# Kernel optimization log

Measured on AMD Instinct MI355X. Metric: run time of the kernel, lower is better.

## Reference

```python
import jax, jax.numpy as jnp
import numpy as np
import math

NUM_BLOCKS = 8
SPARSITY_THRESHOLD = 0.01
HARD_FRAC = 1.0
HIDDEN_SIZE = 1024
HIDDEN_FACTOR = 2
SCALE = 0.02


def _dht1d(x, axis):
    # Discrete Hartley transform along `axis`: sum x * cas(2*pi*k*n/N)
    # cas = cos + sin, equivalently Re(FFT) - Im(FFT).
    F = jnp.fft.fft(x, axis=axis)
    return F.real - F.imag


def dht2d(x):
    # Separable 2D Hartley transform over the spatial axes (1, 2) of (B,H,W,C).
    return _dht1d(_dht1d(x, 1), 2)


def setup_inputs() -> dict:
    key = jax.random.key(0)
    k_x, k_w1, k_b1, k_w2, k_b2 = jax.random.split(key, 5)
    B, N, C = 4, 16384, HIDDEN_SIZE
    bs = C // NUM_BLOCKS                      # 128
    hid = bs * HIDDEN_FACTOR                  # 256
    x = jax.random.normal(k_x, (B, N, C), dtype=jnp.float32)
    w1 = SCALE * jax.random.normal(k_w1, (2, NUM_BLOCKS, bs, hid), dtype=jnp.float32)
    b1 = SCALE * jax.random.normal(k_b1, (2, NUM_BLOCKS, hid), dtype=jnp.float32)
    w2 = SCALE * jax.random.normal(k_w2, (2, NUM_BLOCKS, hid, bs), dtype=jnp.float32)
    b2 = SCALE * jax.random.normal(k_b2, (2, NUM_BLOCKS, bs), dtype=jnp.float32)
    return {"x": x, "w1": w1, "b1": b1, "w2": w2, "b2": b2}


def reference(x, w1, b1, w2, b2):
    bias = x
    B, N, C = x.shape
    H = W = int(math.sqrt(N))
    bs = C // NUM_BLOCKS

    xs = x.reshape(B, H, W, C)
    xs = dht2d(xs)                                    # spatial Hartley domain
    xs = xs.reshape(B, H, W, NUM_BLOCKS, bs)

    kept = int(math.sqrt(H * W) * HARD_FRAC)          # = H when frac == 1
    xk = xs[:, :kept, :kept]                          # (B, kept, kept, nb, bs)

    # Block-diagonal spectral MLP; the source sums contributions from both
    # weight slices w[0] and w[1] with bias b[0].
    o1 = jax.nn.relu(
        jnp.einsum("bxyni,nio->bxyno", xk, w1[0])
        + jnp.einsum("bxyni,nio->bxyno", xk, w1[1])
        + b1[0]
    )                                                 # (B, kept, kept, nb, hid)
    o2k = (
        jnp.einsum("bxyno,noi->bxyni", o1, w2[0])
        + jnp.einsum("bxyno,noi->bxyni", o1, w2[1])
        + b2[0]
    )                                                 # (B, kept, kept, nb, bs)

    o2 = jnp.zeros_like(xs).at[:, :kept, :kept].set(o2k)

    # softshrink
    lam = jnp.float32(SPARSITY_THRESHOLD)
    z = jnp.sign(o2) * jax.nn.relu(jnp.abs(o2) - lam)

    z = z.reshape(B, H, W, C)
    z = dht2d(z) / (H * W)                            # inverse Hartley
    return z.reshape(B, N, C) + bias
```

## Files before the change

### kernel.cpp

```cpp
#include <hip/hip_runtime.h>

typedef unsigned short u16;
typedef unsigned int   u32;
typedef __attribute__((ext_vector_type(8))) short bf16x8;
typedef __attribute__((ext_vector_type(4))) short bf16x4;
typedef __attribute__((ext_vector_type(4))) float f32x4;

#define LAM 0.01f

__device__ __forceinline__ u16 f2bf(float f){
  u32 u = __float_as_uint(f);
  u = u + 0x7FFFu + ((u >> 16) & 1u);
  return (u16)(u >> 16);
}

__device__ __forceinline__ int swz(int row, int k){
  return row*128 + ((((k >> 3) ^ row) & 15) << 3) + (k & 7);
}

#define MFMA16(ac, a, b) ac = __builtin_amdgcn_mfma_f32_16x16x32_bf16((a), (b), (ac), 0, 0, 0)

#define GEMM_STEP(acc, A0,A1,A2,A3, B0,B1,B2,B3) \
  MFMA16(acc[0], A0,B0); MFMA16(acc[1], A0,B1); MFMA16(acc[2], A0,B2); MFMA16(acc[3], A0,B3); \
  MFMA16(acc[4], A1,B0); MFMA16(acc[5], A1,B1); MFMA16(acc[6], A1,B2); MFMA16(acc[7], A1,B3); \
  MFMA16(acc[8], A2,B0); MFMA16(acc[9], A2,B1); MFMA16(acc[10],A2,B2); MFMA16(acc[11],A2,B3); \
  MFMA16(acc[12],A3,B0); MFMA16(acc[13],A3,B1); MFMA16(acc[14],A3,B2); MFMA16(acc[15],A3,B3);

__global__ void k_prep(const float* __restrict__ w1, const float* __restrict__ w2,
                       u16* __restrict__ Mg, u16* __restrict__ W1et, u16* __restrict__ W2et){
  int gid = blockIdx.x * 256 + threadIdx.x;
  if (gid < 16384){
    int i = gid >> 7, j = gid & 127;
    int t = (i * j) & 127;
    float ang = (float)t * 0.04908738521234052f;
    Mg[gid] = f2bf(cosf(ang) + sinf(ang));
  } else if (gid < 16384 + 262144){
    int e = gid - 16384;
    int n = e >> 15, o = (e >> 7) & 255, i = e & 127;
    float v = w1[(n*128 + i)*256 + o] + w1[((8+n)*128 + i)*256 + o];
    W1et[e] = f2bf(v);
  } else {
    int e = gid - (16384 + 262144);
    int n = e >> 15, i = (e >> 8) & 127, o = e & 255;
    float v = w2[(n*256 + o)*128 + i] + w2[((8+n)*256 + o)*128 + i];
    W2et[e] = f2bf(v);
  }
}

__launch_bounds__(256, 2)
__global__ void k_dht_fwd(const float* __restrict__ x, const u16* __restrict__ Mg,
                          u16* __restrict__ Ag){
  __shared__ u16 xt[128*128];
  __shared__ u16 st[128*128];
  int bi = blockIdx.x;
  int n = bi & 7, w = (bi >> 3) & 127, b = bi >> 10;
  int tid = threadIdx.x;
  int lane = tid & 63, wid = tid >> 6;
  int l15 = lane & 15, q = lane >> 4;
  int r0 = (wid >> 1) * 64, c0 = (wid & 1) * 64;

  {
    int c = tid & 127, hg = tid >> 7;
    const float* xb = x + ((b*128)*128 + w)*1024 + n*128 + c;
    for (int it = 0; it < 32; ++it){
      int h0 = (hg + 2*it) * 2;
      float v0 = xb[h0 * 131072];
      float v1 = xb[(h0+1) * 131072];
      u32 pk = (u32)f2bf(v0) | ((u32)f2bf(v1) << 16);
      *(u32*)(&xt[swz(c, h0)]) = pk;
    }
  }
  __syncthreads();

  f32x4 acc[16];
#pragma unroll
  for (int t = 0; t < 16; ++t) acc[t] = f32x4{0.f,0.f,0.f,0.f};

#pragma unroll
  for (int ks = 0; ks < 4; ++ks){
    int kk = ks*32 + q*8;
    bf16x8 a0 = *(const bf16x8*)(Mg + (r0 +  0 + l15)*128 + kk);
    bf16x8 a1 = *(const bf16x8*)(Mg + (r0 + 16 + l15)*128 + kk);
    bf16x8 a2 = *(const bf16x8*)(Mg + (r0 + 32 + l15)*128 + kk);
    bf16x8 a3 = *(const bf16x8*)(Mg + (r0 + 48 + l15)*128 + kk);
    bf16x8 b0 = *(const bf16x8*)(&xt[swz(c0 +  0 + l15, kk)]);
    bf16x8 b1 = *(const bf16x8*)(&xt[swz(c0 + 16 + l15, kk)]);
    bf16x8 b2 = *(const bf16x8*)(&xt[swz(c0 + 32 + l15, kk)]);
    bf16x8 b3 = *(const bf16x8*)(&xt[swz(c0 + 48 + l15, kk)]);
    GEMM_STEP(acc, a0,a1,a2,a3, b0,b1,b2,b3);
  }

#pragma unroll
  for (int i = 0; i < 4; ++i){
    int rb = r0 + 16*i + q*4;
#pragma unroll
    for (int j = 0; j < 4; ++j){
      int col = c0 + 16*j + l15;
      f32x4 v = acc[i*4+j];
      st[swz(rb+0, col)] = f2bf(v.x);
      st[swz(rb+1, col)] = f2bf(v.y);
      st[swz(rb+2, col)] = f2bf(v.z);
      st[swz(rb+3, col)] = f2bf(v.w);
    }
  }
  __syncthreads();
  u16* Aout = Ag + ((b*128)*128 + w)*1024 + n*128;
#pragma unroll
  for (int it = 0; it < 8; ++it){
    int cid = it*256 + tid;
    int row = cid >> 4, cp = cid & 15;
    bf16x8 v = *(const bf16x8*)(&st[row*128 + (((cp ^ row) & 15) << 3)]);
    *(bf16x8*)(Aout + row*131072 + cp*8) = v;
  }
}

__launch_bounds__(256, 2)
__global__ void k_mlp(const u16* __restrict__ Xg, const u16* __restrict__ W1et,
                      const u16* __restrict__ W2et, const u16* __restrict__ Mg,
                      const float* __restrict__ b1g, const float* __restrict__ b2g,
                      u16* __restrict__ Ug){
  __shared__ u16 bufA[128*128];
  __shared__ u16 bufB[128*128];
  int bi = blockIdx.x;
  int n = bi & 7, h = (bi >> 3) & 127, b = bi >> 10;
  int tid = threadIdx.x;
  int lane = tid & 63, wid = tid >> 6;
  int l15 = lane & 15, q = lane >> 4;
  int r0 = (wid >> 1) * 64, c0 = (wid & 1) * 64;

  const u16*  Xbase  = Xg + ((b*128 + h)*128)*1024 + n*128;
  const u16*  W1base = W1et + n*256*128;
  const u16*  W2base = W2et + n*128*256;
  const float* b1base = b1g + n*256;
  const float* b2base = b2g + n*128;

  f32x4 acc2[16], acc1[16];
#pragma unroll
  for (int t = 0; t < 16; ++t) acc2[t] = f32x4{0.f,0.f,0.f,0.f};

  for (int half = 0; half < 2; ++half){
#pragma unroll
    for (int t = 0; t < 16; ++t) acc1[t] = f32x4{0.f,0.f,0.f,0.f};
#pragma unroll
    for (int ks = 0; ks < 4; ++ks){
      int kk = ks*32 + q*8;
      bf16x8 a0 = *(const bf16x8*)(Xbase + (r0 +  0 + l15)*1024 + kk);
      bf16x8 a1 = *(const bf16x8*)(Xbase + (r0 + 16 + l15)*1024 + kk);
      bf16x8 a2 = *(const bf16x8*)(Xbase + (r0 + 32 + l15)*1024 + kk);
      bf16x8 a3 = *(const bf16x8*)(Xbase + (r0 + 48 + l15)*1024 + kk);
      const u16* wb = W1base + (half*128 + c0 + l15)*128 + kk;
      bf16x8 b0 = *(const bf16x8*)(wb);
      bf16x8 b1 = *(const bf16x8*)(wb + 16*128);
      bf16x8 b2 = *(const bf16x8*)(wb + 32*128);
      bf16x8 b3 = *(const bf16x8*)(wb + 48*128);
      GEMM_STEP(acc1, a0,a1,a2,a3, b0,b1,b2,b3);
    }
#pragma unroll
    for (int i = 0; i < 4; ++i){
      int kw = r0 + 16*i + q*4;
#pragma unroll
      for (int j = 0; j < 4; ++j){
        int row = c0 + 16*j + l15;
        f32x4 v = acc1[i*4+j];
        bf16x4 pk;
        pk.x = (short)f2bf(v.x); pk.y = (short)f2bf(v.y);
        pk.z = (short)f2bf(v.z); pk.w = (short)f2bf(v.w);
        *(bf16x4*)(&bufA[swz(row, kw)]) = pk;
      }
    }
    __syncthreads();

#pragma unroll
    for (int t = 0; t < 16; ++t) acc1[t] = f32x4{0.f,0.f,0.f,0.f};
#pragma unroll
    for (int ks = 0; ks < 4; ++ks){
      int kk = ks*32 + q*8;
      bf16x8 a0 = *(const bf16x8*)(&bufA[swz(r0 +  0 + l15, kk)]);
      bf16x8 a1 = *(const bf16x8*)(&bufA[swz(r0 + 16 + l15, kk)]);
      bf16x8 a2 = *(const bf16x8*)(&bufA[swz(r0 + 32 + l15, kk)]);
      bf16x8 a3 = *(const bf16x8*)(&bufA[swz(r0 + 48 + l15, kk)]);
      bf16x8 b0 = *(const bf16x8*)(Mg + (c0 +  0 + l15)*128 + kk);
      bf16x8 b1 = *(const bf16x8*)(Mg + (c0 + 16 + l15)*128 + kk);
      bf16x8 b2 = *(const bf16x8*)(Mg + (c0 + 32 + l15)*128 + kk);
      bf16x8 b3 = *(const bf16x8*)(Mg + (c0 + 48 + l15)*128 + kk);
      GEMM_STEP(acc1, a0,a1,a2,a3, b0,b1,b2,b3);
    }
#pragma unroll
    for (int i = 0; i < 4; ++i){
      int ko = r0 + 16*i + q*4;
      float bs0 = b1base[half*128 + ko + 0];
      float bs1 = b1base[half*128 + ko + 1];
      float bs2 = b1base[half*128 + ko + 2];
      float bs3 = b1base[half*128 + ko + 3];
#pragma unroll
      for (int j = 0; j < 4; ++j){
        int row = c0 + 16*j + l15;
        f32x4 v = acc1[i*4+j];
        bf16x4 pk;
        pk.x = (short)f2bf(fmaxf(v.x + bs0, 0.f));
        pk.y = (short)f2bf(fmaxf(v.y + bs1, 0.f));
        pk.z = (short)f2bf(fmaxf(v.z + bs2, 0.f));
        pk.w = (short)f2bf(fmaxf(v.w + bs3, 0.f));
        *(bf16x4*)(&bufB[swz(row, ko)]) = pk;
      }
    }
    __syncthreads();

#pragma unroll
    for (int ks = 0; ks < 4; ++ks){
      int kk = ks*32 + q*8;
      bf16x8 a0 = *(const bf16x8*)(&bufB[swz(r0 +  0 + l15, kk)]);
      bf16x8 a1 = *(const bf16x8*)(&bufB[swz(r0 + 16 + l15, kk)]);
      bf16x8 a2 = *(const bf16x8*)(&bufB[swz(r0 + 32 + l15, kk)]);
      bf16x8 a3 = *(const bf16x8*)(&bufB[swz(r0 + 48 + l15, kk)]);
      const u16* wb = W2base + (c0 + l15)*256 + half*128 + kk;
      bf16x8 b0 = *(const bf16x8*)(wb);
      bf16x8 b1 = *(const bf16x8*)(wb + 16*256);
      bf16x8 b2 = *(const bf16x8*)(wb + 32*256);
      bf16x8 b3 = *(const bf16x8*)(wb + 48*256);
      GEMM_STEP(acc2, a0,a1,a2,a3, b0,b1,b2,b3);
    }
    __syncthreads();
  }

  {
    float b2v[4];
#pragma unroll
    for (int j = 0; j < 4; ++j) b2v[j] = b2base[c0 + 16*j + l15];
#pragma unroll
    for (int i = 0; i < 4; ++i){
      int kw = r0 + 16*i + q*4;
#pragma unroll
      for (int j = 0; j < 4; ++j){
        int row = c0 + 16*j + l15;
        f32x4 v = acc2[i*4+j];
        float t0 = v.x + b2v[j], t1 = v.y + b2v[j], t2 = v.z + b2v[j], t3 = v.w + b2v[j];
        float m0 = fmaxf(fabsf(t0) - LAM, 0.f);
        float m1 = fmaxf(fabsf(t1) - LAM, 0.f);
        float m2 = fmaxf(fabsf(t2) - LAM, 0.f);
        float m3 = fmaxf(fabsf(t3) - LAM, 0.f);
        bf16x4 pk;
        pk.x = (short)f2bf(t0 >= 0.f ? m0 : -m0);
        pk.y = (short)f2bf(t1 >= 0.f ? m1 : -m1);
        pk.z = (short)f2bf(t2 >= 0.f ? m2 : -m2);
        pk.w = (short)f2bf(t3 >= 0.f ? m3 : -m3);
        *(bf16x4*)(&bufA[swz(row, kw)]) = pk;
      }
    }
  }
  __syncthreads();

#pragma unroll
  for (int t = 0; t < 16; ++t) acc1[t] = f32x4{0.f,0.f,0.f,0.f};
#pragma unroll
  for (int ks = 0; ks < 4; ++ks){
    int kk = ks*32 + q*8;
    bf16x8 a0 = *(const bf16x8*)(Mg + (r0 +  0 + l15)*128 + kk);
    bf16x8 a1 = *(const bf16x8*)(Mg + (r0 + 16 + l15)*128 + kk);
    bf16x8 a2 = *(const bf16x8*)(Mg + (r0 + 32 + l15)*128 + kk);
    bf16x8 a3 = *(const bf16x8*)(Mg + (r0 + 48 + l15)*128 + kk);
    bf16x8 b0 = *(const bf16x8*)(&bufA[swz(c0 +  0 + l15, kk)]);
    bf16x8 b1 = *(const bf16x8*)(&bufA[swz(c0 + 16 + l15, kk)]);
    bf16x8 b2 = *(const bf16x8*)(&bufA[swz(c0 + 32 + l15, kk)]);
    bf16x8 b3 = *(const bf16x8*)(&bufA[swz(c0 + 48 + l15, kk)]);
    GEMM_STEP(acc1, a0,a1,a2,a3, b0,b1,b2,b3);
  }
#pragma unroll
  for (int i = 0; i < 4; ++i){
    int rb = r0 + 16*i + q*4;
#pragma unroll
    for (int j = 0; j < 4; ++j){
      int col = c0 + 16*j + l15;
      f32x4 v = acc1[i*4+j];
      bufB[swz(rb+0, col)] = f2bf(v.x);
      bufB[swz(rb+1, col)] = f2bf(v.y);
      bufB[swz(rb+2, col)] = f2bf(v.z);
      bufB[swz(rb+3, col)] = f2bf(v.w);
    }
  }
  __syncthreads();
  u16* Ubase = Ug + ((b*128 + h)*128)*1024 + n*128;
#pragma unroll
  for (int it = 0; it < 8; ++it){
    int cid = it*256 + tid;
    int row = cid >> 4, cp = cid & 15;
    bf16x8 v = *(const bf16x8*)(&bufB[row*128 + (((cp ^ row) & 15) << 3)]);
    *(bf16x8*)(Ubase + row*1024 + cp*8) = v;
  }
}

__launch_bounds__(256, 2)
__global__ void k_dht_inv(const u16* __restrict__ Ug, const u16* __restrict__ Mg,
                          const float* __restrict__ x, float* __restrict__ out){
  __shared__ u16 ut[128*128];
  int bi = blockIdx.x;
  int n = bi & 7, w = (bi >> 3) & 127, b = bi >> 10;
  int tid = threadIdx.x;
  int lane = tid & 63, wid = tid >> 6;
  int l15 = lane & 15, q = lane >> 4;
  int r0 = (wid >> 1) * 64, c0 = (wid & 1) * 64;

  {
    int cp = (tid & 63) * 2, hb = (tid >> 6) * 2;
    const u16* Ub = Ug + ((b*128)*128 + w)*1024 + n*128;
#pragma unroll
    for (int it = 0; it < 16; ++it){
      int h0 = hb + it*8;
      u32 d0 = *(const u32*)(Ub + h0*131072 + cp);
      u32 d1 = *(const u32*)(Ub + (h0+1)*131072 + cp);
      u32 lo = (d0 & 0xFFFFu) | ((d1 & 0xFFFFu) << 16);
      u32 hi = (d0 >> 16) | (d1 & 0xFFFF0000u);
      *(u32*)(&ut[swz(cp,   h0)]) = lo;
      *(u32*)(&ut[swz(cp+1, h0)]) = hi;
    }
  }
  __syncthreads();

  f32x4 acc[16];
#pragma unroll
  for (int t = 0; t < 16; ++t) acc[t] = f32x4{0.f,0.f,0.f,0.f};

#pragma unroll
  for (int ks = 0; ks < 4; ++ks){
    int kk = ks*32 + q*8;
    bf16x8 a0 = *(const bf16x8*)(Mg + (r0 +  0 + l15)*128 + kk);
    bf16x8 a1 = *(const bf16x8*)(Mg + (r0 + 16 + l15)*128 + kk);
    bf16x8 a2 = *(const bf16x8*)(Mg + (r0 + 32 + l15)*128 + kk);
    bf16x8 a3 = *(const bf16x8*)(Mg + (r0 + 48 + l15)*128 + kk);
    bf16x8 b0 = *(const bf16x8*)(&ut[swz(c0 +  0 + l15, kk)]);
    bf16x8 b1 = *(const bf16x8*)(&ut[swz(c0 + 16 + l15, kk)]);
    bf16x8 b2 = *(const bf16x8*)(&ut[swz(c0 + 32 + l15, kk)]);
    bf16x8 b3 = *(const bf16x8*)(&ut[swz(c0 + 48 + l15, kk)]);
    GEMM_STEP(acc, a0,a1,a2,a3, b0,b1,b2,b3);
  }

  const float s = 1.f / 16384.f;
  int gbase = ((b*128)*128 + w)*1024 + n*128;
#pragma unroll
  for (int i = 0; i < 4; ++i){
    int hh = r0 + 16*i + q*4;
#pragma unroll
    for (int j = 0; j < 4; ++j){
      int cc = c0 + 16*j + l15;
      f32x4 v = acc[i*4+j];
      int i0 = gbase + (hh+0)*131072 + cc; out[i0] = v.x * s + x[i0];
      int i1 = gbase + (hh+1)*131072 + cc; out[i1] = v.y * s + x[i1];
      int i2 = gbase + (hh+2)*131072 + cc; out[i2] = v.z * s + x[i2];
      int i3 = gbase + (hh+3)*131072 + cc; out[i3] = v.w * s + x[i3];
    }
  }
}

extern "C" void kernel_launch(void* const* d_in, const int* in_sizes, int n_in,
                              void* d_out, int out_size, void* d_ws, size_t ws_size,
                              hipStream_t stream) {
  const float* x  = (const float*)d_in[0];
  const float* w1 = (const float*)d_in[1];
  const float* b1 = (const float*)d_in[2];
  const float* w2 = (const float*)d_in[3];
  const float* b2 = (const float*)d_in[4];
  float* out = (float*)d_out;

  u16* Ag   = (u16*)d_out;
  u16* W1et = (u16*)((char*)d_out + 267386880);
  u16* W2et = (u16*)((char*)d_out + 267911168);
  u16* Ug   = (u16*)d_ws;
  u16* Mg   = (u16*)((char*)d_ws + 134217728);

  k_prep<<<2112, 256, 0, stream>>>(w1, w2, Mg, W1et, W2et);
  k_dht_fwd<<<4096, 256, 0, stream>>>(x, Mg, Ag);
  k_mlp<<<4096, 256, 0, stream>>>(Ag, W1et, W2et, Mg, b1, b2, Ug);
  k_dht_inv<<<4096, 256, 0, stream>>>(Ug, Mg, x, out);
}
```

Before: 1.102 ms.

## Add nontemporal loads/stores, reuse LDS buffer, raise occupancy, hoist MLP input loads

```diff
diff --git a/kernel.cpp b/kernel.cpp
--- a/kernel.cpp
+++ b/kernel.cpp
@@ -47,11 +47,10 @@
   }
 }
 
-__launch_bounds__(256, 2)
+__launch_bounds__(256, 4)
 __global__ void k_dht_fwd(const float* __restrict__ x, const u16* __restrict__ Mg,
                           u16* __restrict__ Ag){
   __shared__ u16 xt[128*128];
-  __shared__ u16 st[128*128];
   int bi = blockIdx.x;
   int n = bi & 7, w = (bi >> 3) & 127, b = bi >> 10;
   int tid = threadIdx.x;
@@ -64,8 +63,8 @@
     const float* xb = x + ((b*128)*128 + w)*1024 + n*128 + c;
     for (int it = 0; it < 32; ++it){
       int h0 = (hg + 2*it) * 2;
-      float v0 = xb[h0 * 131072];
-      float v1 = xb[(h0+1) * 131072];
+      float v0 = __builtin_nontemporal_load(xb + h0 * 131072);
+      float v1 = __builtin_nontemporal_load(xb + (h0+1) * 131072);
       u32 pk = (u32)f2bf(v0) | ((u32)f2bf(v1) << 16);
       *(u32*)(&xt[swz(c, h0)]) = pk;
     }
@@ -89,6 +88,7 @@
     bf16x8 b3 = *(const bf16x8*)(&xt[swz(c0 + 48 + l15, kk)]);
     GEMM_STEP(acc, a0,a1,a2,a3, b0,b1,b2,b3);
   }
+  __syncthreads();
 
 #pragma unroll
   for (int i = 0; i < 4; ++i){
@@ -97,10 +97,10 @@
     for (int j = 0; j < 4; ++j){
       int col = c0 + 16*j + l15;
       f32x4 v = acc[i*4+j];
-      st[swz(rb+0, col)] = f2bf(v.x);
-      st[swz(rb+1, col)] = f2bf(v.y);
-      st[swz(rb+2, col)] = f2bf(v.z);
-      st[swz(rb+3, col)] = f2bf(v.w);
+      xt[swz(rb+0, col)] = f2bf(v.x);
+      xt[swz(rb+1, col)] = f2bf(v.y);
+      xt[swz(rb+2, col)] = f2bf(v.z);
+      xt[swz(rb+3, col)] = f2bf(v.w);
     }
   }
   __syncthreads();
@@ -109,8 +109,8 @@
   for (int it = 0; it < 8; ++it){
     int cid = it*256 + tid;
     int row = cid >> 4, cp = cid & 15;
-    bf16x8 v = *(const bf16x8*)(&st[row*128 + (((cp ^ row) & 15) << 3)]);
-    *(bf16x8*)(Aout + row*131072 + cp*8) = v;
+    bf16x8 v = *(const bf16x8*)(&xt[row*128 + (((cp ^ row) & 15) << 3)]);
+    __builtin_nontemporal_store(v, (bf16x8*)(Aout + row*131072 + cp*8));
   }
 }
 
@@ -134,6 +134,15 @@
   const float* b1base = b1g + n*256;
   const float* b2base = b2g + n*128;
 
+  bf16x8 xa[16];
+#pragma unroll
+  for (int ks = 0; ks < 4; ++ks){
+    int kk = ks*32 + q*8;
+#pragma unroll
+    for (int g = 0; g < 4; ++g)
+      xa[ks*4+g] = *(const bf16x8*)(Xbase + (r0 + 16*g + l15)*1024 + kk);
+  }
+
   f32x4 acc2[16], acc1[16];
 #pragma unroll
   for (int t = 0; t < 16; ++t) acc2[t] = f32x4{0.f,0.f,0.f,0.f};
@@ -144,16 +153,12 @@
 #pragma unroll
     for (int ks = 0; ks < 4; ++ks){
       int kk = ks*32 + q*8;
-      bf16x8 a0 = *(const bf16x8*)(Xbase + (r0 +  0 + l15)*1024 + kk);
-      bf16x8 a1 = *(const bf16x8*)(Xbase + (r0 + 16 + l15)*1024 + kk);
-      bf16x8 a2 = *(const bf16x8*)(Xbase + (r0 + 32 + l15)*1024 + kk);
-      bf16x8 a3 = *(const bf16x8*)(Xbase + (r0 + 48 + l15)*1024 + kk);
       const u16* wb = W1base + (half*128 + c0 + l15)*128 + kk;
       bf16x8 b0 = *(const bf16x8*)(wb);
       bf16x8 b1 = *(const bf16x8*)(wb + 16*128);
       bf16x8 b2 = *(const bf16x8*)(wb + 32*128);
       bf16x8 b3 = *(const bf16x8*)(wb + 48*128);
-      GEMM_STEP(acc1, a0,a1,a2,a3, b0,b1,b2,b3);
+      GEMM_STEP(acc1, xa[ks*4+0], xa[ks*4+1], xa[ks*4+2], xa[ks*4+3], b0,b1,b2,b3);
     }
 #pragma unroll
     for (int i = 0; i < 4; ++i){
@@ -285,11 +290,11 @@
     int cid = it*256 + tid;
     int row = cid >> 4, cp = cid & 15;
     bf16x8 v = *(const bf16x8*)(&bufB[row*128 + (((cp ^ row) & 15) << 3)]);
-    *(bf16x8*)(Ubase + row*1024 + cp*8) = v;
-  }
-}
-
-__launch_bounds__(256, 2)
+    __builtin_nontemporal_store(v, (bf16x8*)(Ubase + row*1024 + cp*8));
+  }
+}
+
+__launch_bounds__(256, 4)
 __global__ void k_dht_inv(const u16* __restrict__ Ug, const u16* __restrict__ Mg,
                           const float* __restrict__ x, float* __restrict__ out){
   __shared__ u16 ut[128*128];
@@ -306,8 +311,8 @@
 #pragma unroll
     for (int it = 0; it < 16; ++it){
       int h0 = hb + it*8;
-      u32 d0 = *(const u32*)(Ub + h0*131072 + cp);
-      u32 d1 = *(const u32*)(Ub + (h0+1)*131072 + cp);
+      u32 d0 = __builtin_nontemporal_load((const u32*)(Ub + h0*131072 + cp));
+      u32 d1 = __builtin_nontemporal_load((const u32*)(Ub + (h0+1)*131072 + cp));
       u32 lo = (d0 & 0xFFFFu) | ((d1 & 0xFFFFu) << 16);
       u32 hi = (d0 >> 16) | (d1 & 0xFFFF0000u);
       *(u32*)(&ut[swz(cp,   h0)]) = lo;
@@ -343,10 +348,18 @@
     for (int j = 0; j < 4; ++j){
       int cc = c0 + 16*j + l15;
       f32x4 v = acc[i*4+j];
-      int i0 = gbase + (hh+0)*131072 + cc; out[i0] = v.x * s + x[i0];
-      int i1 = gbase + (hh+1)*131072 + cc; out[i1] = v.y * s + x[i1];
-      int i2 = gbase + (hh+2)*131072 + cc; out[i2] = v.z * s + x[i2];
-      int i3 = gbase + (hh+3)*131072 + cc; out[i3] = v.w * s + x[i3];
+      int i0 = gbase + (hh+0)*131072 + cc;
+      int i1 = gbase + (hh+1)*131072 + cc;
+      int i2 = gbase + (hh+2)*131072 + cc;
+      int i3 = gbase + (hh+3)*131072 + cc;
+      float x0 = __builtin_nontemporal_load(x + i0);
+      float x1 = __builtin_nontemporal_load(x + i1);
+      float x2 = __builtin_nontemporal_load(x + i2);
+      float x3 = __builtin_nontemporal_load(x + i3);
+      __builtin_nontemporal_store(v.x * s + x0, out + i0);
+      __builtin_nontemporal_store(v.y * s + x1, out + i1);
+      __builtin_nontemporal_store(v.z * s + x2, out + i2);
+      __builtin_nontemporal_store(v.w * s + x3, out + i3);
     }
   }
 }
```

New measurement: 1.072 ms. 2.7% less time.
